# Performance work log

Hardware: AMD Instinct MI355X
Metric: run time of the kernel (lower is better)

## Reference

```python
import jax, jax.numpy as jnp
import numpy as np

D = 768  # n_dim


def setup_inputs() -> dict:
    key = jax.random.key(0)
    ks = jax.random.split(key, 9)
    B, S = 4, 4096
    s = 0.02
    return {
        "x": jax.random.normal(ks[0], (B, S, D), dtype=jnp.float32),
        "Wq": jax.random.normal(ks[1], (D, D), dtype=jnp.float32) * s,
        "bq": jax.random.normal(ks[2], (D,), dtype=jnp.float32) * s,
        "Wk": jax.random.normal(ks[3], (D, D), dtype=jnp.float32) * s,
        "bk": jax.random.normal(ks[4], (D,), dtype=jnp.float32) * s,
        "Wv": jax.random.normal(ks[5], (D, D), dtype=jnp.float32) * s,
        "bv": jax.random.normal(ks[6], (D,), dtype=jnp.float32) * s,
        "Wc": jax.random.normal(ks[7], (D, D), dtype=jnp.float32) * s,
        "bc": jax.random.normal(ks[8], (D,), dtype=jnp.float32) * s,
    }


def reference(x, Wq, bq, Wk, bk, Wv, bv, Wc, bc):
    # Faithful to the source's executed math (its head-reshape and masked_fill
    # results are discarded): single-'head' full-dim attention, NO causal mask,
    # scale = n_dim**-0.5, then a transpose(1,2).reshape element permutation.
    B, S, nd = x.shape
    q = jnp.einsum('bsd,ed->bse', x, Wq) + bq  # nn.Linear: x @ W.T + b
    k = jnp.einsum('bsd,ed->bse', x, Wk) + bk
    v = jnp.einsum('bsd,ed->bse', x, Wv) + bv
    att = jnp.einsum('bqd,bkd->bqk', q, k) * (nd ** -0.5)  # [B,S,S]
    att = jax.nn.softmax(att, axis=-1)  # no mask (bug preserved)
    y = jnp.einsum('bqk,bkd->bqd', att, v)  # [B,S,D]
    y = jnp.transpose(y, (0, 2, 1)).reshape(B, S, nd)  # element permutation (bug preserved)
    return jnp.einsum('bsd,ed->bse', y, Wc) + bc
```

## Files before the change

### kernel.cpp

```cpp
#include <hip/hip_runtime.h>
#include <stdint.h>


typedef __bf16 bf16;
typedef __bf16 bf16x4 __attribute__((ext_vector_type(4)));
typedef __bf16 bf16x8 __attribute__((ext_vector_type(8)));
typedef float f32x4 __attribute__((ext_vector_type(4)));

#define OFF_Q    0L
#define OFF_K    25165824L
#define OFF_VT   50331648L
#define OFF_W    75497472L
#define OFF_B    80216064L
#define OFF_FLAG 80222208L
#define OFF_L    80223232L
#define OFF_ATT  80289792L
#define ATT_B    33554432L
#define SD       3145728L

#define M_PLAIN  0
#define M_TRANSC 1
#define M_EXPSUM 2
#define M_DIVL   3

__device__ __forceinline__ void glds16(const void* g, void* s) {
  __builtin_amdgcn_global_load_lds((const __attribute__((address_space(1))) void*)g,
                                   (__attribute__((address_space(3))) void*)s, 16, 0, 0);
}

#define SBAR()  do { asm volatile("" ::: "memory"); __builtin_amdgcn_s_barrier(); \
                     asm volatile("" ::: "memory"); } while (0)
#define LGKM0() do { asm volatile("s_waitcnt lgkmcnt(0)" ::: "memory"); \
                     __builtin_amdgcn_sched_barrier(0); } while (0)

#define MFMA_AB(ac, aa, bb) do { \
  if (MODE == M_TRANSC) { \
    ac = __builtin_amdgcn_mfma_f32_16x16x32_bf16((aa)[0], (bb)[0], ac, 0, 0, 0); \
    ac = __builtin_amdgcn_mfma_f32_16x16x32_bf16((aa)[1], (bb)[1], ac, 0, 0, 0); \
  } else { \
    ac = __builtin_amdgcn_mfma_f32_16x16x32_bf16((bb)[0], (aa)[0], ac, 0, 0, 0); \
    ac = __builtin_amdgcn_mfma_f32_16x16x32_bf16((bb)[1], (aa)[1], ac, 0, 0, 0); \
  } \
} while (0)

__global__ void sniff_dtype(const uint16_t* __restrict__ x, int* __restrict__ flag)
{
  const int t = threadIdx.x;
  int bad = 0;
  for (int i = t; i < 4096; i += 256) {
    const int e = (x[2 * i] >> 7) & 0xFF;
    bad |= (e >= 0xE0);
  }
  __shared__ int s;
  if (t == 0) s = 0;
  __syncthreads();
  if (bad) s = 1;
  __syncthreads();
  if (t == 0) *flag = s;
}

__device__ __forceinline__ void norm8(const void* __restrict__ src, bf16* __restrict__ dst,
                                      long i, long n8, int f)
{
  if (i >= n8) return;
  bf16x8 o;
  if (f) {
    const float4 a = ((const float4*)src)[2 * i];
    const float4 b = ((const float4*)src)[2 * i + 1];
    o[0] = (bf16)a.x; o[1] = (bf16)a.y; o[2] = (bf16)a.z; o[3] = (bf16)a.w;
    o[4] = (bf16)b.x; o[5] = (bf16)b.y; o[6] = (bf16)b.z; o[7] = (bf16)b.w;
  } else {
    o = ((const bf16x8*)src)[i];
  }
  ((bf16x8*)dst)[i] = o;
}

__global__ void normalize_all(const void* x,
                              const void* w0, const void* b0, const void* w1, const void* b1,
                              const void* w2, const void* b2, const void* w3, const void* b3,
                              bf16* __restrict__ xn, bf16* __restrict__ Wn,
                              bf16* __restrict__ bn, float* __restrict__ lsum,
                              const int* __restrict__ flag)
{
  const int t = threadIdx.x;
  const int f = *flag;
  int b = blockIdx.x;
  if (b < 6144) { norm8(x, xn, (long)b * 256 + t, 1572864L, f); return; }
  b -= 6144;
  if (b < 1152) {
    const int w = b / 288;
    const void* s = (w == 0) ? w0 : (w == 1) ? w1 : (w == 2) ? w2 : w3;
    norm8(s, Wn + (long)w * 589824L, (long)(b % 288) * 256 + t, 73728L, f);
    return;
  }
  b -= 1152;
  if (b < 4) {
    const void* s = (b == 0) ? b0 : (b == 1) ? b1 : (b == 2) ? b2 : b3;
    norm8(s, bn + (long)b * 768L, (long)t, 96L, f);
    return;
  }
  b -= 4;
  lsum[(long)b * 256 + t] = 0.f;
}

template <int MODE>
__launch_bounds__(512, 2)
__global__ void gemm256(const bf16* __restrict__ A, int lda, long strideA,
                        const bf16* __restrict__ Bm, int ldb, long strideB,
                        void* __restrict__ Cv, int ldc, long strideC,
                        int K, const bf16* __restrict__ bias, float alpha,
                        const int* __restrict__ oflag, float* __restrict__ lsum)
{
  __shared__ bf16 lds[65536];
  A  += (long)blockIdx.z * strideA;
  Bm += (long)blockIdx.z * strideB;
  if (MODE == M_EXPSUM || MODE == M_DIVL) lsum += (long)blockIdx.z * 4096L;

  const int gx = gridDim.x;
  int lin = blockIdx.y * gx + blockIdx.x;
  const int cpx = (gx * gridDim.y) >> 3;
  lin = (lin & 7) * cpx + (lin >> 3);
  const long m0 = (long)(lin / gx) * 256, n0 = (long)(lin % gx) * 256;

  const int tid = threadIdx.x;
  const int wv = tid >> 6, lane = tid & 63;
  const int lr = lane & 15, quad = lane >> 4;
  const int wm = (wv >> 2) << 7;
  const int wn = (wv & 3) << 6;

  f32x4 acc[8][4];
  const f32x4 zero = {0.f, 0.f, 0.f, 0.f};
#pragma unroll
  for (int i = 0; i < 8; ++i)
#pragma unroll
    for (int j = 0; j < 4; ++j) acc[i][j] = zero;

  const int rowid = (wv << 4) + (lane >> 3);
  const int colsw = ((lane & 7) ^ ((lane >> 3) & 7)) << 3;
  const long lda8 = 8L * lda, ldb8 = 8L * ldb;
  const bf16* paL = A + (m0 + rowid) * (long)lda + colsw;
  const bf16* paH = paL + 128L * lda;
  const bf16* pbL = Bm + (n0 + rowid) * (long)ldb + colsw;
  const bf16* pbH = pbL + 128L * ldb;

  auto STG = [&](const bf16* src, long ld8, int tbuf, int reg) {
    bf16* d = lds + (tbuf << 15) + (reg << 13) + (wv << 10);
    glds16(src, d);
    glds16(src + ld8, d + 512);
  };

  const int regA = 1 + ((wv >> 2) << 1);
  const int regB = wv & 2;
  const int aoff = lr << 6;
  const int boff = ((wv & 1) << 12) + (lr << 6);
  const int xo  = (lr & 7) << 3;
  const int ok0 = (quad << 3) ^ xo;
  const int ok1 = (32 + (quad << 3)) ^ xo;

  const int nt = K >> 6;

  STG(pbL, ldb8, 0, 0); STG(paL, lda8, 0, 1);
  STG(pbH, ldb8, 0, 2); STG(paH, lda8, 0, 3);
  asm volatile("s_waitcnt vmcnt(4)" ::: "memory");
  STG(pbL + 64, ldb8, 1, 0); STG(paL + 64, lda8, 1, 1);
  STG(pbH + 64, ldb8, 1, 2);
  asm volatile("s_waitcnt vmcnt(6)" ::: "memory");
  SBAR();

  for (int t = 0; t < nt; ++t) {
    const int buf = t & 1;
    const long k64 = (long)t << 6;
    const bf16* LA = lds + (buf << 15) + (regA << 13) + aoff;
    const bf16* LB = lds + (buf << 15) + (regB << 13) + boff;
    bf16x8 aL[4][2], aH[4][2], bF[4][2];

#pragma unroll
    for (int i = 0; i < 4; ++i) {
      aL[i][0] = *(const bf16x8*)(LA + i * 1024 + ok0);
      aL[i][1] = *(const bf16x8*)(LA + i * 1024 + ok1);
    }
#pragma unroll
    for (int j = 0; j < 4; ++j) {
      bF[j][0] = *(const bf16x8*)(LB + j * 1024 + ok0);
      bF[j][1] = *(const bf16x8*)(LB + j * 1024 + ok1);
    }
    if (t + 1 < nt) STG(paH + k64 + 64, lda8, (t + 1) & 1, 3);
    SBAR();
    LGKM0();
    __builtin_amdgcn_s_setprio(1);
#pragma unroll
    for (int i = 0; i < 4; ++i)
#pragma unroll
      for (int j = 0; j < 2; ++j) MFMA_AB(acc[i][j], aL[i], bF[j]);
    __builtin_amdgcn_s_setprio(0);
    SBAR();

#pragma unroll
    for (int i = 0; i < 4; ++i) {
      aH[i][0] = *(const bf16x8*)(LA + (4 + i) * 1024 + ok0);
      aH[i][1] = *(const bf16x8*)(LA + (4 + i) * 1024 + ok1);
    }
    if (t + 2 < nt) STG(pbL + k64 + 128, ldb8, buf, 0);
    SBAR();
    LGKM0();
    __builtin_amdgcn_s_setprio(1);
#pragma unroll
    for (int i = 0; i < 4; ++i)
#pragma unroll
      for (int j = 0; j < 2; ++j) MFMA_AB(acc[4 + i][j], aH[i], bF[j]);
    __builtin_amdgcn_s_setprio(0);
    SBAR();

    if (t + 2 < nt) STG(paL + k64 + 128, lda8, buf, 1);
    SBAR();
    __builtin_amdgcn_s_setprio(1);
#pragma unroll
    for (int i = 0; i < 4; ++i)
#pragma unroll
      for (int j = 0; j < 2; ++j) MFMA_AB(acc[i][2 + j], aL[i], bF[2 + j]);
    __builtin_amdgcn_s_setprio(0);
    SBAR();

    if (t + 2 < nt) STG(pbH + k64 + 128, ldb8, buf, 2);
    SBAR();
    __builtin_amdgcn_s_setprio(1);
#pragma unroll
    for (int i = 0; i < 4; ++i)
#pragma unroll
      for (int j = 0; j < 2; ++j) MFMA_AB(acc[4 + i][2 + j], aH[i], bF[2 + j]);
    __builtin_amdgcn_s_setprio(0);
    if (t + 2 < nt) asm volatile("s_waitcnt vmcnt(6)" ::: "memory");
    else            asm volatile("s_waitcnt vmcnt(0)" ::: "memory");
    SBAR();
  }

  if (MODE == M_TRANSC) {
#pragma unroll
    for (int j = 0; j < 4; ++j) {
      const long col = n0 + wn + j * 16 + lr;
      const float bv = (float)bias[col];
#pragma unroll
      for (int i = 0; i < 8; ++i) {
        const long row = m0 + wm + i * 16 + quad * 4;
        bf16x4 v4;
#pragma unroll
        for (int r = 0; r < 4; ++r) v4[r] = (bf16)((acc[i][j][r] + bv) * alpha);
        *(bf16x4*)((bf16*)Cv + (long)blockIdx.z * strideC + col * (long)ldc + row) = v4;
      }
    }
    return;
  }

  const int outf32 = (MODE == M_PLAIN) && (oflag != nullptr) && (*oflag != 0);
  long colb[4];
  f32x4 addv[4];
#pragma unroll
  for (int j = 0; j < 4; ++j) {
    colb[j] = n0 + wn + j * 16 + quad * 4;
    if (MODE == M_PLAIN) {
      const bf16x4 bb = *(const bf16x4*)(bias + colb[j]);
#pragma unroll
      for (int r = 0; r < 4; ++r) addv[j][r] = (float)bb[r];
    } else if (MODE == M_DIVL) {
      const f32x4 lv = *(const f32x4*)(lsum + colb[j]);
#pragma unroll
      for (int r = 0; r < 4; ++r) addv[j][r] = 1.0f / lv[r];
    }
  }
#pragma unroll
  for (int i = 0; i < 8; ++i) {
    const long row = m0 + wm + i * 16 + lr;
    char* rowp = (char*)Cv + ((long)blockIdx.z * strideC + row * (long)ldc) * (outf32 ? 4 : 2);
    float rsum = 0.f;
#pragma unroll
    for (int j = 0; j < 4; ++j) {
      f32x4 v;
#pragma unroll
      for (int r = 0; r < 4; ++r) {
        float t = acc[i][j][r];
        if (MODE == M_PLAIN)       t = (t + addv[j][r]) * alpha;
        else if (MODE == M_EXPSUM) t = __expf(t);
        else if (MODE == M_DIVL)   t = t * addv[j][r];
        v[r] = t;
      }
      if (MODE == M_PLAIN && outf32) {
        *(f32x4*)(rowp + colb[j] * 4) = v;
      } else {
        bf16x4 v4;
#pragma unroll
        for (int r = 0; r < 4; ++r) v4[r] = (bf16)v[r];
        if (MODE == M_EXPSUM) {
#pragma unroll
          for (int r = 0; r < 4; ++r) rsum += (float)v4[r];
        }
        *(bf16x4*)(rowp + colb[j] * 2) = v4;
      }
    }
    if (MODE == M_EXPSUM) {
      rsum += __shfl_xor(rsum, 16);
      rsum += __shfl_xor(rsum, 32);
      if (quad == 0) atomicAdd(&lsum[row], rsum);
    }
  }
}

extern "C" void kernel_launch(void* const* d_in, const int* in_sizes, int n_in,
                              void* d_out, int out_size, void* d_ws, size_t ws_size,
                              hipStream_t stream)
{
  (void)in_sizes; (void)n_in; (void)out_size;
  char* ws = (char*)d_ws;

  if (ws_size < (size_t)(OFF_ATT + ATT_B)) return;
  const size_t avail = ws_size - (size_t)OFF_ATT;
  int group = (int)(avail / (size_t)ATT_B);
  group = group >= 4 ? 4 : (group >= 2 ? 2 : 1);

  bf16*  q    = (bf16*)(ws + OFF_Q);
  bf16*  k    = (bf16*)(ws + OFF_K);
  bf16*  vT2  = (bf16*)(ws + OFF_VT);
  bf16*  Wn   = (bf16*)(ws + OFF_W);
  bf16*  bn   = (bf16*)(ws + OFF_B);
  int*   flg  = (int*)(ws + OFF_FLAG);
  float* lbase= (float*)(ws + OFF_L);
  bf16*  att  = (bf16*)(ws + OFF_ATT);
  bf16*  xn   = att;

  dim3 blk(256, 1, 1), blk2(512, 1, 1);
  const float qs = 0.03608439182435161f;

  sniff_dtype<<<1, blk, 0, stream>>>((const uint16_t*)d_in[0], flg);
  normalize_all<<<7364, blk, 0, stream>>>(d_in[0],
                                          d_in[1], d_in[2], d_in[3], d_in[4],
                                          d_in[5], d_in[6], d_in[7], d_in[8],
                                          xn, Wn, bn, lbase, flg);

  dim3 gproj(3, 64, 1);
  gemm256<M_PLAIN><<<gproj, blk2, 0, stream>>>(xn, 768, 0, Wn + 0 * 589824L, 768, 0,
                                               q, 768, 0, 768, bn + 0, qs, nullptr, nullptr);
  gemm256<M_PLAIN><<<gproj, blk2, 0, stream>>>(xn, 768, 0, Wn + 1 * 589824L, 768, 0,
                                               k, 768, 0, 768, bn + 768, 1.f, nullptr, nullptr);
  gemm256<M_TRANSC><<<gproj, blk2, 0, stream>>>(xn, 768, 0, Wn + 2 * 589824L, 768, 0,
                                                vT2, 16384, 0, 768, bn + 1536, 1.f, nullptr, nullptr);

  for (int g = 0; g < 4; g += group) {
    dim3 gs(16, 16, group);
    gemm256<M_EXPSUM><<<gs, blk2, 0, stream>>>(q + g * SD, 768, SD, k + g * SD, 768, SD,
                                               att, 4096, 16777216L, 768, nullptr, 1.f,
                                               nullptr, lbase + g * 4096L);
    dim3 gpv(16, 3, group);
    gemm256<M_DIVL><<<gpv, blk2, 0, stream>>>(vT2 + g * 4096L, 16384, 4096L,
                                              att, 4096, 16777216L,
                                              q + g * SD, 4096, SD, 4096, nullptr, 1.f,
                                              nullptr, lbase + g * 4096L);
  }

  dim3 gout(3, 64, 1);
  gemm256<M_PLAIN><<<gout, blk2, 0, stream>>>(q, 768, 0, Wn + 3 * 589824L, 768, 0,
                                              d_out, 768, 0, 768, bn + 2304, 1.f, flg, nullptr);
}
```

Before: 486.5 us.

## Fuse Q/K/V projections into one GEMM and fold dtype sniff into normalize

Merges the three separate projection GEMM launches into one launch over a 9x64 grid against the concatenated weight matrix, routing each column block to q, k, or transposed v output. The dtype-detection kernel is removed and its check is done per block inside normalize_all. It also adds a custom 16x16-grid block swizzle for the attention score GEMM to improve L2 locality. These changes cut launch count and tail effects, in exchange for a per-block branch between transposed and plain MFMA paths and a redundant sniff in every normalize block.

New measurement: 605.6 us. +24.5%, slower.

```diff
diff --git a/kernel.cpp b/kernel.cpp
--- a/kernel.cpp
+++ b/kernel.cpp
@@ -17,11 +17,13 @@
 #define OFF_ATT  80289792L
 #define ATT_B    33554432L
 #define SD       3145728L
+#define KOFF     12582912L
+#define VTOFF    25165824L
 
 #define M_PLAIN  0
-#define M_TRANSC 1
 #define M_EXPSUM 2
 #define M_DIVL   3
+#define M_QKV    4
 
 __device__ __forceinline__ void glds16(const void* g, void* s) {
   __builtin_amdgcn_global_load_lds((const __attribute__((address_space(1))) void*)g,
@@ -33,31 +35,24 @@
 #define LGKM0() do { asm volatile("s_waitcnt lgkmcnt(0)" ::: "memory"); \
                      __builtin_amdgcn_sched_barrier(0); } while (0)
 
-#define MFMA_AB(ac, aa, bb) do { \
-  if (MODE == M_TRANSC) { \
-    ac = __builtin_amdgcn_mfma_f32_16x16x32_bf16((aa)[0], (bb)[0], ac, 0, 0, 0); \
-    ac = __builtin_amdgcn_mfma_f32_16x16x32_bf16((aa)[1], (bb)[1], ac, 0, 0, 0); \
+#define MFMA2(ac, aa, bb) do { \
+  ac = __builtin_amdgcn_mfma_f32_16x16x32_bf16((bb)[0], (aa)[0], ac, 0, 0, 0); \
+  ac = __builtin_amdgcn_mfma_f32_16x16x32_bf16((bb)[1], (aa)[1], ac, 0, 0, 0); \
+} while (0)
+#define MFMA2T(ac, aa, bb) do { \
+  ac = __builtin_amdgcn_mfma_f32_16x16x32_bf16((aa)[0], (bb)[0], ac, 0, 0, 0); \
+  ac = __builtin_amdgcn_mfma_f32_16x16x32_bf16((aa)[1], (bb)[1], ac, 0, 0, 0); \
+} while (0)
+
+#define CLUSTER(I0, JO, AF) do { \
+  if (trsw) { \
+    _Pragma("unroll") for (int i = 0; i < 4; ++i) \
+      _Pragma("unroll") for (int j = 0; j < 2; ++j) MFMA2T(acc[(I0)+i][(JO)+j], AF[i], bF[(JO)+j]); \
   } else { \
-    ac = __builtin_amdgcn_mfma_f32_16x16x32_bf16((bb)[0], (aa)[0], ac, 0, 0, 0); \
-    ac = __builtin_amdgcn_mfma_f32_16x16x32_bf16((bb)[1], (aa)[1], ac, 0, 0, 0); \
+    _Pragma("unroll") for (int i = 0; i < 4; ++i) \
+      _Pragma("unroll") for (int j = 0; j < 2; ++j) MFMA2(acc[(I0)+i][(JO)+j], AF[i], bF[(JO)+j]); \
   } \
 } while (0)
-
-__global__ void sniff_dtype(const uint16_t* __restrict__ x, int* __restrict__ flag)
-{
-  const int t = threadIdx.x;
-  int bad = 0;
-  for (int i = t; i < 4096; i += 256) {
-    const int e = (x[2 * i] >> 7) & 0xFF;
-    bad |= (e >= 0xE0);
-  }
-  __shared__ int s;
-  if (t == 0) s = 0;
-  __syncthreads();
-  if (bad) s = 1;
-  __syncthreads();
-  if (t == 0) *flag = s;
-}
 
 __device__ __forceinline__ void norm8(const void* __restrict__ src, bf16* __restrict__ dst,
                                       long i, long n8, int f)
@@ -80,11 +75,22 @@
                               const void* w2, const void* b2, const void* w3, const void* b3,
                               bf16* __restrict__ xn, bf16* __restrict__ Wn,
                               bf16* __restrict__ bn, float* __restrict__ lsum,
-                              const int* __restrict__ flag)
+                              int* __restrict__ flagOut)
 {
   const int t = threadIdx.x;
-  const int f = *flag;
+  __shared__ int sflag;
+  if (t == 0) sflag = 0;
+  __syncthreads();
+  {
+    const uint16_t* xu = (const uint16_t*)x;
+    const int e = (xu[2 * t] >> 7) & 0xFF;
+    if (e >= 0xE0) sflag = 1;
+  }
+  __syncthreads();
+  const int f = sflag;
   int b = blockIdx.x;
+  if (b == 0 && t == 0) *flagOut = f;
+
   if (b < 6144) { norm8(x, xn, (long)b * 256 + t, 1572864L, f); return; }
   b -= 6144;
   if (b < 1152) {
@@ -116,11 +122,19 @@
   Bm += (long)blockIdx.z * strideB;
   if (MODE == M_EXPSUM || MODE == M_DIVL) lsum += (long)blockIdx.z * 4096L;
 
-  const int gx = gridDim.x;
-  int lin = blockIdx.y * gx + blockIdx.x;
-  const int cpx = (gx * gridDim.y) >> 3;
-  lin = (lin & 7) * cpx + (lin >> 3);
-  const long m0 = (long)(lin / gx) * 256, n0 = (long)(lin % gx) * 256;
+  const int gx = gridDim.x, gy = gridDim.y;
+  const int lin = blockIdx.y * gx + blockIdx.x;
+  int nlin;
+  if (gx == 16 && gy == 16) {
+    const int c = lin & 7, i = lin >> 3;
+    nlin = (((c >> 1) << 2) + (i >> 3)) * 16 + ((c & 1) << 3) + (i & 7);
+  } else {
+    const int cpx = (gx * gy) >> 3;
+    nlin = (lin & 7) * cpx + (lin >> 3);
+  }
+  const long m0 = (long)(nlin / gx) * 256, n0 = (long)(nlin % gx) * 256;
+
+  const bool trsw = (MODE == M_QKV) && (n0 >= 1536);
 
   const int tid = threadIdx.x;
   const int wv = tid >> 6, lane = tid & 63;
@@ -188,10 +202,7 @@
     SBAR();
     LGKM0();
     __builtin_amdgcn_s_setprio(1);
-#pragma unroll
-    for (int i = 0; i < 4; ++i)
-#pragma unroll
-      for (int j = 0; j < 2; ++j) MFMA_AB(acc[i][j], aL[i], bF[j]);
+    CLUSTER(0, 0, aL);
     __builtin_amdgcn_s_setprio(0);
     SBAR();
 
@@ -204,48 +215,67 @@
     SBAR();
     LGKM0();
     __builtin_amdgcn_s_setprio(1);
-#pragma unroll
-    for (int i = 0; i < 4; ++i)
-#pragma unroll
-      for (int j = 0; j < 2; ++j) MFMA_AB(acc[4 + i][j], aH[i], bF[j]);
+    CLUSTER(4, 0, aH);
     __builtin_amdgcn_s_setprio(0);
     SBAR();
 
     if (t + 2 < nt) STG(paL + k64 + 128, lda8, buf, 1);
     SBAR();
     __builtin_amdgcn_s_setprio(1);
-#pragma unroll
-    for (int i = 0; i < 4; ++i)
-#pragma unroll
-      for (int j = 0; j < 2; ++j) MFMA_AB(acc[i][2 + j], aL[i], bF[2 + j]);
+    CLUSTER(0, 2, aL);
     __builtin_amdgcn_s_setprio(0);
     SBAR();
 
     if (t + 2 < nt) STG(pbH + k64 + 128, ldb8, buf, 2);
     SBAR();
     __builtin_amdgcn_s_setprio(1);
-#pragma unroll
-    for (int i = 0; i < 4; ++i)
-#pragma unroll
-      for (int j = 0; j < 2; ++j) MFMA_AB(acc[4 + i][2 + j], aH[i], bF[2 + j]);
+    CLUSTER(4, 2, aH);
     __builtin_amdgcn_s_setprio(0);
     if (t + 2 < nt) asm volatile("s_waitcnt vmcnt(6)" ::: "memory");
     else            asm volatile("s_waitcnt vmcnt(0)" ::: "memory");
     SBAR();
   }
 
-  if (MODE == M_TRANSC) {
-#pragma unroll
-    for (int j = 0; j < 4; ++j) {
-      const long col = n0 + wn + j * 16 + lr;
-      const float bv = (float)bias[col];
+  if (MODE == M_QKV) {
+    if (trsw) {
+      bf16* dst = (bf16*)Cv + VTOFF;
+#pragma unroll
+      for (int j = 0; j < 4; ++j) {
+        const long col = n0 + wn + j * 16 + lr;
+        const float bv = (float)bias[col];
+#pragma unroll
+        for (int i = 0; i < 8; ++i) {
+          const long row = m0 + wm + i * 16 + quad * 4;
+          bf16x4 v4;
+#pragma unroll
+          for (int r = 0; r < 4; ++r) v4[r] = (bf16)(acc[i][j][r] + bv);
+          *(bf16x4*)(dst + (col - 1536L) * 16384L + row) = v4;
+        }
+      }
+    } else {
+      const int seg = (n0 >= 768);
+      bf16* dst = (bf16*)Cv + (long)seg * KOFF;
+      const float al = seg ? 1.f : alpha;
+      long coll[4];
+      f32x4 addv[4];
+#pragma unroll
+      for (int j = 0; j < 4; ++j) {
+        const long coln = n0 + wn + j * 16 + quad * 4;
+        const bf16x4 bb = *(const bf16x4*)(bias + coln);
+#pragma unroll
+        for (int r = 0; r < 4; ++r) addv[j][r] = (float)bb[r];
+        coll[j] = coln - (long)seg * 768L;
+      }
 #pragma unroll
       for (int i = 0; i < 8; ++i) {
-        const long row = m0 + wm + i * 16 + quad * 4;
-        bf16x4 v4;
-#pragma unroll
-        for (int r = 0; r < 4; ++r) v4[r] = (bf16)((acc[i][j][r] + bv) * alpha);
-        *(bf16x4*)((bf16*)Cv + (long)blockIdx.z * strideC + col * (long)ldc + row) = v4;
+        const long row = m0 + wm + i * 16 + lr;
+#pragma unroll
+        for (int j = 0; j < 4; ++j) {
+          bf16x4 v4;
+#pragma unroll
+          for (int r = 0; r < 4; ++r) v4[r] = (bf16)((acc[i][j][r] + addv[j][r]) * al);
+          *(bf16x4*)(dst + row * 768L + coll[j]) = v4;
+        }
       }
     }
     return;
@@ -317,7 +347,6 @@
   group = group >= 4 ? 4 : (group >= 2 ? 2 : 1);
 
   bf16*  q    = (bf16*)(ws + OFF_Q);
-  bf16*  k    = (bf16*)(ws + OFF_K);
   bf16*  vT2  = (bf16*)(ws + OFF_VT);
   bf16*  Wn   = (bf16*)(ws + OFF_W);
   bf16*  bn   = (bf16*)(ws + OFF_B);
@@ -325,31 +354,27 @@
   float* lbase= (float*)(ws + OFF_L);
   bf16*  att  = (bf16*)(ws + OFF_ATT);
   bf16*  xn   = att;
+  (void)vT2;
 
   dim3 blk(256, 1, 1), blk2(512, 1, 1);
   const float qs = 0.03608439182435161f;
 
-  sniff_dtype<<<1, blk, 0, stream>>>((const uint16_t*)d_in[0], flg);
   normalize_all<<<7364, blk, 0, stream>>>(d_in[0],
                                           d_in[1], d_in[2], d_in[3], d_in[4],
                                           d_in[5], d_in[6], d_in[7], d_in[8],
                                           xn, Wn, bn, lbase, flg);
 
-  dim3 gproj(3, 64, 1);
-  gemm256<M_PLAIN><<<gproj, blk2, 0, stream>>>(xn, 768, 0, Wn + 0 * 589824L, 768, 0,
-                                               q, 768, 0, 768, bn + 0, qs, nullptr, nullptr);
-  gemm256<M_PLAIN><<<gproj, blk2, 0, stream>>>(xn, 768, 0, Wn + 1 * 589824L, 768, 0,
-                                               k, 768, 0, 768, bn + 768, 1.f, nullptr, nullptr);
-  gemm256<M_TRANSC><<<gproj, blk2, 0, stream>>>(xn, 768, 0, Wn + 2 * 589824L, 768, 0,
-                                                vT2, 16384, 0, 768, bn + 1536, 1.f, nullptr, nullptr);
+  dim3 gqkv(9, 64, 1);
+  gemm256<M_QKV><<<gqkv, blk2, 0, stream>>>(xn, 768, 0, Wn, 768, 0,
+                                            q, 768, 0, 768, bn, qs, nullptr, nullptr);
 
   for (int g = 0; g < 4; g += group) {
     dim3 gs(16, 16, group);
-    gemm256<M_EXPSUM><<<gs, blk2, 0, stream>>>(q + g * SD, 768, SD, k + g * SD, 768, SD,
+    gemm256<M_EXPSUM><<<gs, blk2, 0, stream>>>(q + g * SD, 768, SD, q + KOFF + g * SD, 768, SD,
                                                att, 4096, 16777216L, 768, nullptr, 1.f,
                                                nullptr, lbase + g * 4096L);
     dim3 gpv(16, 3, group);
-    gemm256<M_DIVL><<<gpv, blk2, 0, stream>>>(vT2 + g * 4096L, 16384, 4096L,
+    gemm256<M_DIVL><<<gpv, blk2, 0, stream>>>(q + VTOFF + g * 4096L, 16384, 4096L,
                                               att, 4096, 16777216L,
                                               q + g * SD, 4096, SD, 4096, nullptr, 1.f,
                                               nullptr, lbase + g * 4096L);
```
